# Kernel optimization log

Hardware: AMD Instinct MI355X
Metric: run time of the kernel (lower is better)

## Reference

```python
import jax, jax.numpy as jnp
import numpy as np

NUM_USERS = 100000
NUM_RATINGS = 5
EMBED_DIM = 64
ATT_DIM = 16
B, G, L, S = 16384, 8, 50, 32


def setup_inputs() -> dict:
    key = jax.random.key(0)
    ks = jax.random.split(key, 16)
    inp = {
        # forward args (int / bool constants)
        "nodes": jax.random.randint(ks[0], (B, G), 0, NUM_USERS),
        "history_u": jax.random.randint(ks[1], (B, L), 0, NUM_USERS),
        "history_r": jax.random.randint(ks[2], (B, L), 0, NUM_RATINGS),
        "history_mask": jax.random.randint(ks[3], (B, L), 0, 2).astype(bool).at[:, 0].set(True),
        "social_adj": jax.random.randint(ks[4], (B, S), 0, NUM_USERS),
        "social_mask": jax.random.randint(ks[5], (B, S), 0, 2).astype(bool).at[:, 0].set(True),
        # learned parameters
        "features": jax.random.normal(ks[6], (NUM_USERS, EMBED_DIM), jnp.float32) * 0.02,
        "r_embed": jax.random.normal(ks[7], (NUM_RATINGS, EMBED_DIM), jnp.float32) * 0.02,
        "wg1": jax.random.normal(ks[8], (EMBED_DIM, ATT_DIM), jnp.float32) / np.sqrt(EMBED_DIM),
        "bg1": jnp.zeros((ATT_DIM,), jnp.float32),
        "wg2": jax.random.normal(ks[9], (ATT_DIM, 1), jnp.float32) / np.sqrt(ATT_DIM),
        "bg2": jnp.zeros((1,), jnp.float32),
        "w1": jax.random.normal(ks[10], (2 * EMBED_DIM, EMBED_DIM), jnp.float32) / np.sqrt(2 * EMBED_DIM),
        "b1": jnp.zeros((EMBED_DIM,), jnp.float32),
    }
    return inp


def _masked_mean(x, mask):
    # x: [B, N, D], mask: [B, N] float -> [B, D]
    denom = jnp.maximum(mask.sum(axis=1, keepdims=True), 1.0)
    return (x * mask[..., None]).sum(axis=1) / denom


def reference(nodes, history_u, history_r, history_mask, social_adj, social_mask,
              features, r_embed, wg1, bg1, wg2, bg2, w1, b1):
    dt = features.dtype
    # --- Group_Embedding: attention pooling over member embeddings ---
    members = features[nodes]                              # [B, G, D] gather
    h = jnp.tanh(members @ wg1 + bg1)                      # [B, G, 16]
    logits = (h @ wg2 + bg2)[..., 0]                       # [B, G]
    alpha = jax.nn.softmax(logits, axis=-1)
    self_feats = jnp.einsum('bg,bgd->bd', alpha, members)  # [B, D]

    # --- aggregator: ragged history (item+rating) + social neighbor means ---
    hm = history_mask.astype(dt)
    hist = features[history_u] + r_embed[history_r]        # [B, L, D] gather
    hist_mean = _masked_mean(hist, hm)                     # [B, D]

    sm = social_mask.astype(dt)
    soc_mean = _masked_mean(features[social_adj], sm)      # [B, D]

    neigh_feats = 0.5 * (hist_mean + soc_mean)             # [B, D]

    # --- concat -> linear -> relu ---
    combined = jnp.concatenate([self_feats, neigh_feats], axis=1)  # [B, 2D]
    return jax.nn.relu(combined @ w1 + b1)                 # [B, D]
```

## Files before the change

### kernel.cpp

```cpp
#include <hip/hip_runtime.h>
#include <cstdint>
#include <cstddef>

#define NUSERS 100000
#define BB 16384

static __device__ __forceinline__ unsigned short f2bf(float x) {
    unsigned u = __float_as_uint(x);
    u += 0x7FFF + ((u >> 16) & 1);
    return (unsigned short)(u >> 16);
}
static __device__ __forceinline__ float4 bf4_to_f4(ushort4 h) {
    float4 r;
    r.x = __uint_as_float((unsigned)h.x << 16);
    r.y = __uint_as_float((unsigned)h.y << 16);
    r.z = __uint_as_float((unsigned)h.z << 16);
    r.w = __uint_as_float((unsigned)h.w << 16);
    return r;
}

__global__ __launch_bounds__(256) void k0_scores(
    const float* __restrict__ features, const float* __restrict__ wg1,
    const float* __restrict__ bg1, const float* __restrict__ wg2,
    const float* __restrict__ bg2, float* __restrict__ Q,
    unsigned short* __restrict__ fbf)
{
    __shared__ float frow[16 * 68];
    __shared__ float wg1t[16 * 68];
    const int tid = threadIdx.x;
    const int blk = blockIdx.x;

    const float4 v = ((const float4*)(features + (size_t)blk * 1024))[tid];
    {
        const int row = tid >> 4, q = tid & 15;
        *(float4*)&frow[row * 68 + q * 4] = v;
    }
    {
        const float4 w = ((const float4*)wg1)[tid];
        const int d = tid >> 2, k0 = (tid & 3) * 4;
        wg1t[(k0 + 0) * 68 + d] = w.x;
        wg1t[(k0 + 1) * 68 + d] = w.y;
        wg1t[(k0 + 2) * 68 + d] = w.z;
        wg1t[(k0 + 3) * 68 + d] = w.w;
    }
    {
        ushort4 o;
        o.x = f2bf(v.x); o.y = f2bf(v.y); o.z = f2bf(v.z); o.w = f2bf(v.w);
        *(ushort4*)(fbf + (size_t)blk * 1024 + tid * 4) = o;
    }
    __syncthreads();

    const int k = tid & 15, ul = tid >> 4;
    float x = bg1[k];
    #pragma unroll
    for (int d4 = 0; d4 < 16; ++d4) {
        const float4 f  = *(const float4*)&frow[ul * 68 + d4 * 4];
        const float4 wv = *(const float4*)&wg1t[k * 68 + d4 * 4];
        x += f.x * wv.x + f.y * wv.y + f.z * wv.z + f.w * wv.w;
    }
    float xx = fminf(fmaxf(x, -9.f), 9.f);
    float e2 = __expf(2.f * xx);
    float th = (e2 - 1.f) / (e2 + 1.f);
    float t = th * wg2[k];
    t += __shfl_xor(t, 1);
    t += __shfl_xor(t, 2);
    t += __shfl_xor(t, 4);
    t += __shfl_xor(t, 8);
    if (k == 0) Q[blk * 16 + ul] = t + bg2[0];
}

__global__ __launch_bounds__(256) void k1_fuse(
    const int* __restrict__ nodes, const int* __restrict__ hist_u,
    const int* __restrict__ hist_r, const int* __restrict__ hist_m,
    const int* __restrict__ soc_a, const int* __restrict__ soc_m,
    const unsigned short* __restrict__ fbf, const float* __restrict__ r_embed,
    const float* __restrict__ Q, const float* __restrict__ w1,
    const float* __restrict__ b1, float* __restrict__ out)
{
    __shared__ int   lcomp[4][96];
    __shared__ float wcomp[4][96];
    __shared__ float combs[4][128];

    const int tid = threadIdx.x;
    const int lane = tid & 63;
    const int wv = tid >> 6;
    const int e = blockIdx.x * 4 + wv;
    const int sub = lane & 15;
    const int grp = lane >> 4;
    const char* fb = (const char*)fbf;

    lcomp[wv][lane] = 0;
    wcomp[wv][lane] = 0.f;
    if (lane < 32) { lcomp[wv][64 + lane] = 0; wcomp[wv][64 + lane] = 0.f; }

    const float4* re4p = (const float4*)r_embed;
    const float4 re0 = re4p[0 * 16 + sub];
    const float4 re1 = re4p[1 * 16 + sub];
    const float4 re2 = re4p[2 * 16 + sub];
    const float4 re3 = re4p[3 * 16 + sub];
    const float4 re4 = re4p[4 * 16 + sub];

    int nd = (lane < 8) ? nodes[e * 8 + lane] : 0;
    int hu = 0, hr = 0, hmv = 0;
    if (lane < 50) {
        hu  = hist_u[e * 50 + lane];
        hr  = hist_r[e * 50 + lane];
        hmv = hist_m[e * 50 + lane];
    }
    int sa = 0, sk = 0;
    if (lane < 32) {
        sa = soc_a[e * 32 + lane];
        sk = soc_m[e * 32 + lane];
    }

    uint64_t hb = __ballot(hmv != 0);
    const int hc = (int)__popcll(hb);
    int hrank = (int)__popcll(hb & ((1ull << lane) - 1));

    uint64_t sbm = __ballot(sk != 0);
    const int scn = (int)__popcll(sbm);
    int srank = (int)__popcll(sbm & ((1ull << lane) - 1));

    const float ih = 1.f / (float)hc;
    const float is = 1.f / (float)scn;
    const float hw = 0.5f * ih;
    const float sw = 0.5f * is;

    if (hmv) { lcomp[wv][hrank] = hu << 7; wcomp[wv][hrank] = hw; }
    if (sk)  { lcomp[wv][hc + srank] = sa << 7; wcomp[wv][hc + srank] = sw; }

    const int c0 = (int)__popcll(__ballot(hmv && hr == 0));
    const int c1 = (int)__popcll(__ballot(hmv && hr == 1));
    const int c2 = (int)__popcll(__ballot(hmv && hr == 2));
    const int c3 = (int)__popcll(__ballot(hmv && hr == 3));
    const int c4 = (int)__popcll(__ballot(hmv && hr == 4));

    float sc = (lane < 8) ? Q[nd] : -1e30f;
    float mx = sc;
    mx = fmaxf(mx, __shfl_xor(mx, 1));
    mx = fmaxf(mx, __shfl_xor(mx, 2));
    mx = fmaxf(mx, __shfl_xor(mx, 4));
    float ex = __expf(sc - mx);
    float sm = ex;
    sm += __shfl_xor(sm, 1);
    sm += __shfl_xor(sm, 2);
    sm += __shfl_xor(sm, 4);
    float al = ex / sm;

    int   pkA = lcomp[wv][lane];
    int   pkB = lcomp[wv][64 + (lane & 31)];
    float wgA = wcomp[wv][lane];
    float wgB = wcomp[wv][64 + (lane & 31)];
    const int n = hc + scn;

    float4 sf4;
    {
        float a0 = __shfl(al, grp);
        int   u0 = __shfl(nd, grp);
        float a1 = __shfl(al, 4 + grp);
        int   u1 = __shfl(nd, 4 + grp);
        const float4 v0 = bf4_to_f4(*(const ushort4*)(fb + ((unsigned)u0 << 7) + sub * 8));
        const float4 v1 = bf4_to_f4(*(const ushort4*)(fb + ((unsigned)u1 << 7) + sub * 8));
        sf4.x = a0 * v0.x + a1 * v1.x;
        sf4.y = a0 * v0.y + a1 * v1.y;
        sf4.z = a0 * v0.z + a1 * v1.z;
        sf4.w = a0 * v0.w + a1 * v1.w;
    }

    float4 nb4 = {0.f, 0.f, 0.f, 0.f};
    for (int base = 0; base < n; base += 16) {
        #pragma unroll
        for (int j = 0; j < 4; ++j) {
            const int cbase = base + j * 4;
            int off; float w;
            if (cbase < 64) {
                off = __shfl(pkA, cbase + grp);
                w   = __shfl(wgA, cbase + grp);
            } else {
                off = __shfl(pkB, cbase - 64 + grp);
                w   = __shfl(wgB, cbase - 64 + grp);
            }
            const float4 v = bf4_to_f4(*(const ushort4*)(fb + (unsigned)off + sub * 8));
            nb4.x += w * v.x; nb4.y += w * v.y;
            nb4.z += w * v.z; nb4.w += w * v.w;
        }
    }

#define XRED(v4)                                            \
    v4.x += __shfl_xor(v4.x, 16); v4.x += __shfl_xor(v4.x, 32); \
    v4.y += __shfl_xor(v4.y, 16); v4.y += __shfl_xor(v4.y, 32); \
    v4.z += __shfl_xor(v4.z, 16); v4.z += __shfl_xor(v4.z, 32); \
    v4.w += __shfl_xor(v4.w, 16); v4.w += __shfl_xor(v4.w, 32);
    XRED(sf4)
    XRED(nb4)
#undef XRED

    float f0 = hw * (float)c0, f1 = hw * (float)c1, f2 = hw * (float)c2,
          f3 = hw * (float)c3, f4 = hw * (float)c4;
    nb4.x += f0 * re0.x + f1 * re1.x + f2 * re2.x + f3 * re3.x + f4 * re4.x;
    nb4.y += f0 * re0.y + f1 * re1.y + f2 * re2.y + f3 * re3.y + f4 * re4.y;
    nb4.z += f0 * re0.z + f1 * re1.z + f2 * re2.z + f3 * re3.z + f4 * re4.z;
    nb4.w += f0 * re0.w + f1 * re1.w + f2 * re2.w + f3 * re3.w + f4 * re4.w;

    if (grp == 0) *(float4*)&combs[wv][sub * 4] = sf4;
    if (grp == 1) *(float4*)&combs[wv][64 + sub * 4] = nb4;

    const int col = lane;
    float y = b1[col];
    #pragma unroll 8
    for (int k4 = 0; k4 < 32; ++k4) {
        const float4 c = *(const float4*)&combs[wv][k4 * 4];
        y += c.x * w1[(k4 * 4 + 0) * 64 + col]
           + c.y * w1[(k4 * 4 + 1) * 64 + col]
           + c.z * w1[(k4 * 4 + 2) * 64 + col]
           + c.w * w1[(k4 * 4 + 3) * 64 + col];
    }
    out[(size_t)e * 64 + col] = fmaxf(y, 0.f);
}

extern "C" void kernel_launch(void* const* d_in, const int* in_sizes, int n_in,
                              void* d_out, int out_size, void* d_ws, size_t ws_size,
                              hipStream_t stream)
{
    const int*   nodes    = (const int*)d_in[0];
    const int*   hu       = (const int*)d_in[1];
    const int*   hr       = (const int*)d_in[2];
    const int*   hm       = (const int*)d_in[3];
    const int*   sa       = (const int*)d_in[4];
    const int*   smk      = (const int*)d_in[5];
    const float* features = (const float*)d_in[6];
    const float* r_embed  = (const float*)d_in[7];
    const float* wg1      = (const float*)d_in[8];
    const float* bg1      = (const float*)d_in[9];
    const float* wg2      = (const float*)d_in[10];
    const float* bg2      = (const float*)d_in[11];
    const float* w1       = (const float*)d_in[12];
    const float* b1       = (const float*)d_in[13];
    float* out = (float*)d_out;

    float*          Q    = (float*)d_ws;
    unsigned short* fbf  = (unsigned short*)(Q + 131072);

    k0_scores<<<NUSERS / 16, 256, 0, stream>>>(features, wg1, bg1, wg2, bg2, Q, fbf);
    k1_fuse<<<BB / 4, 256, 0, stream>>>(nodes, hu, hr, hm, sa, smk,
                                        fbf, r_embed, Q, w1, b1, out);
}
```

Baseline: 139.7 us.

## Fuse score precompute into gather kernel and read fp32 features directly

```diff
diff --git a/kernel.cpp b/kernel.cpp
--- a/kernel.cpp
+++ b/kernel.cpp
@@ -2,39 +2,32 @@
 #include <cstdint>
 #include <cstddef>
 
-#define NUSERS 100000
 #define BB 16384
 
-static __device__ __forceinline__ unsigned short f2bf(float x) {
-    unsigned u = __float_as_uint(x);
-    u += 0x7FFF + ((u >> 16) & 1);
-    return (unsigned short)(u >> 16);
-}
-static __device__ __forceinline__ float4 bf4_to_f4(ushort4 h) {
-    float4 r;
-    r.x = __uint_as_float((unsigned)h.x << 16);
-    r.y = __uint_as_float((unsigned)h.y << 16);
-    r.z = __uint_as_float((unsigned)h.z << 16);
-    r.w = __uint_as_float((unsigned)h.w << 16);
-    return r;
-}
-
-__global__ __launch_bounds__(256) void k0_scores(
-    const float* __restrict__ features, const float* __restrict__ wg1,
-    const float* __restrict__ bg1, const float* __restrict__ wg2,
-    const float* __restrict__ bg2, float* __restrict__ Q,
-    unsigned short* __restrict__ fbf)
+__global__ __launch_bounds__(256) void k_fused(
+    const int* __restrict__ nodes, const int* __restrict__ hist_u,
+    const int* __restrict__ hist_r, const int* __restrict__ hist_m,
+    const int* __restrict__ soc_a, const int* __restrict__ soc_m,
+    const float* __restrict__ features, const float* __restrict__ r_embed,
+    const float* __restrict__ wg1, const float* __restrict__ bg1,
+    const float* __restrict__ wg2, const float* __restrict__ bg2,
+    const float* __restrict__ w1, const float* __restrict__ b1,
+    float* __restrict__ out)
 {
-    __shared__ float frow[16 * 68];
     __shared__ float wg1t[16 * 68];
-    const int tid = threadIdx.x;
-    const int blk = blockIdx.x;
-
-    const float4 v = ((const float4*)(features + (size_t)blk * 1024))[tid];
-    {
-        const int row = tid >> 4, q = tid & 15;
-        *(float4*)&frow[row * 68 + q * 4] = v;
-    }
+    __shared__ float mrow[4][8 * 68];
+    __shared__ int   lcomp[4][96];
+    __shared__ float wcomp[4][96];
+    __shared__ float combs[4][128];
+
+    const int tid  = threadIdx.x;
+    const int lane = tid & 63;
+    const int wv   = tid >> 6;
+    const int e    = blockIdx.x * 4 + wv;
+    const int sub  = lane & 15;
+    const int grp  = lane >> 4;
+    const char* fB = (const char*)features;
+
     {
         const float4 w = ((const float4*)wg1)[tid];
         const int d = tid >> 2, k0 = (tid & 3) * 4;
@@ -43,51 +36,6 @@
         wg1t[(k0 + 2) * 68 + d] = w.z;
         wg1t[(k0 + 3) * 68 + d] = w.w;
     }
-    {
-        ushort4 o;
-        o.x = f2bf(v.x); o.y = f2bf(v.y); o.z = f2bf(v.z); o.w = f2bf(v.w);
-        *(ushort4*)(fbf + (size_t)blk * 1024 + tid * 4) = o;
-    }
-    __syncthreads();
-
-    const int k = tid & 15, ul = tid >> 4;
-    float x = bg1[k];
-    #pragma unroll
-    for (int d4 = 0; d4 < 16; ++d4) {
-        const float4 f  = *(const float4*)&frow[ul * 68 + d4 * 4];
-        const float4 wv = *(const float4*)&wg1t[k * 68 + d4 * 4];
-        x += f.x * wv.x + f.y * wv.y + f.z * wv.z + f.w * wv.w;
-    }
-    float xx = fminf(fmaxf(x, -9.f), 9.f);
-    float e2 = __expf(2.f * xx);
-    float th = (e2 - 1.f) / (e2 + 1.f);
-    float t = th * wg2[k];
-    t += __shfl_xor(t, 1);
-    t += __shfl_xor(t, 2);
-    t += __shfl_xor(t, 4);
-    t += __shfl_xor(t, 8);
-    if (k == 0) Q[blk * 16 + ul] = t + bg2[0];
-}
-
-__global__ __launch_bounds__(256) void k1_fuse(
-    const int* __restrict__ nodes, const int* __restrict__ hist_u,
-    const int* __restrict__ hist_r, const int* __restrict__ hist_m,
-    const int* __restrict__ soc_a, const int* __restrict__ soc_m,
-    const unsigned short* __restrict__ fbf, const float* __restrict__ r_embed,
-    const float* __restrict__ Q, const float* __restrict__ w1,
-    const float* __restrict__ b1, float* __restrict__ out)
-{
-    __shared__ int   lcomp[4][96];
-    __shared__ float wcomp[4][96];
-    __shared__ float combs[4][128];
-
-    const int tid = threadIdx.x;
-    const int lane = tid & 63;
-    const int wv = tid >> 6;
-    const int e = blockIdx.x * 4 + wv;
-    const int sub = lane & 15;
-    const int grp = lane >> 4;
-    const char* fb = (const char*)fbf;
 
     lcomp[wv][lane] = 0;
     wcomp[wv][lane] = 0.f;
@@ -126,8 +74,8 @@
     const float hw = 0.5f * ih;
     const float sw = 0.5f * is;
 
-    if (hmv) { lcomp[wv][hrank] = hu << 7; wcomp[wv][hrank] = hw; }
-    if (sk)  { lcomp[wv][hc + srank] = sa << 7; wcomp[wv][hc + srank] = sw; }
+    if (hmv) { lcomp[wv][hrank] = hu << 8; wcomp[wv][hrank] = hw; }
+    if (sk)  { lcomp[wv][hc + srank] = sa << 8; wcomp[wv][hc + srank] = sw; }
 
     const int c0 = (int)__popcll(__ballot(hmv && hr == 0));
     const int c1 = (int)__popcll(__ballot(hmv && hr == 1));
@@ -135,37 +83,63 @@
     const int c3 = (int)__popcll(__ballot(hmv && hr == 3));
     const int c4 = (int)__popcll(__ballot(hmv && hr == 4));
 
-    float sc = (lane < 8) ? Q[nd] : -1e30f;
-    float mx = sc;
-    mx = fmaxf(mx, __shfl_xor(mx, 1));
-    mx = fmaxf(mx, __shfl_xor(mx, 2));
-    mx = fmaxf(mx, __shfl_xor(mx, 4));
-    float ex = __expf(sc - mx);
-    float sm = ex;
-    sm += __shfl_xor(sm, 1);
-    sm += __shfl_xor(sm, 2);
-    sm += __shfl_xor(sm, 4);
-    float al = ex / sm;
+    const int u0 = __shfl(nd, grp);
+    const int u1 = __shfl(nd, 4 + grp);
+    const float4 v0 = *(const float4*)(fB + ((unsigned)u0 << 8) + sub * 16);
+    const float4 v1 = *(const float4*)(fB + ((unsigned)u1 << 8) + sub * 16);
+    *(float4*)&mrow[wv][grp * 68 + sub * 4]       = v0;
+    *(float4*)&mrow[wv][(4 + grp) * 68 + sub * 4] = v1;
+
+    __syncthreads();
+
+    float h0, h1;
+    {
+        const int k = sub;
+        const float bk = bg1[k];
+        h0 = bk; h1 = bk;
+        #pragma unroll
+        for (int d4 = 0; d4 < 16; ++d4) {
+            const float4 wk = *(const float4*)&wg1t[k * 68 + d4 * 4];
+            const float4 m0 = *(const float4*)&mrow[wv][grp * 68 + d4 * 4];
+            const float4 m1 = *(const float4*)&mrow[wv][(4 + grp) * 68 + d4 * 4];
+            h0 += m0.x * wk.x + m0.y * wk.y + m0.z * wk.z + m0.w * wk.w;
+            h1 += m1.x * wk.x + m1.y * wk.y + m1.z * wk.z + m1.w * wk.w;
+        }
+        const float wk2 = wg2[k];
+        float x0 = fminf(fmaxf(h0, -9.f), 9.f);
+        float x1 = fminf(fmaxf(h1, -9.f), 9.f);
+        float e20 = __expf(2.f * x0), e21 = __expf(2.f * x1);
+        h0 = (e20 - 1.f) / (e20 + 1.f) * wk2;
+        h1 = (e21 - 1.f) / (e21 + 1.f) * wk2;
+        h0 += __shfl_xor(h0, 1); h1 += __shfl_xor(h1, 1);
+        h0 += __shfl_xor(h0, 2); h1 += __shfl_xor(h1, 2);
+        h0 += __shfl_xor(h0, 4); h1 += __shfl_xor(h1, 4);
+        h0 += __shfl_xor(h0, 8); h1 += __shfl_xor(h1, 8);
+    }
+    const float bg2v = bg2[0];
+    const float l0 = h0 + bg2v;
+    const float l1 = h1 + bg2v;
+
+    float mx = fmaxf(l0, l1);
+    mx = fmaxf(mx, __shfl_xor(mx, 16));
+    mx = fmaxf(mx, __shfl_xor(mx, 32));
+    float e0 = __expf(l0 - mx), e1 = __expf(l1 - mx);
+    float s = e0 + e1;
+    s += __shfl_xor(s, 16);
+    s += __shfl_xor(s, 32);
+    const float a0 = e0 / s, a1 = e1 / s;
+
+    float4 sf4;
+    sf4.x = a0 * v0.x + a1 * v1.x;
+    sf4.y = a0 * v0.y + a1 * v1.y;
+    sf4.z = a0 * v0.z + a1 * v1.z;
+    sf4.w = a0 * v0.w + a1 * v1.w;
 
     int   pkA = lcomp[wv][lane];
     int   pkB = lcomp[wv][64 + (lane & 31)];
     float wgA = wcomp[wv][lane];
     float wgB = wcomp[wv][64 + (lane & 31)];
     const int n = hc + scn;
-
-    float4 sf4;
-    {
-        float a0 = __shfl(al, grp);
-        int   u0 = __shfl(nd, grp);
-        float a1 = __shfl(al, 4 + grp);
-        int   u1 = __shfl(nd, 4 + grp);
-        const float4 v0 = bf4_to_f4(*(const ushort4*)(fb + ((unsigned)u0 << 7) + sub * 8));
-        const float4 v1 = bf4_to_f4(*(const ushort4*)(fb + ((unsigned)u1 << 7) + sub * 8));
-        sf4.x = a0 * v0.x + a1 * v1.x;
-        sf4.y = a0 * v0.y + a1 * v1.y;
-        sf4.z = a0 * v0.z + a1 * v1.z;
-        sf4.w = a0 * v0.w + a1 * v1.w;
-    }
 
     float4 nb4 = {0.f, 0.f, 0.f, 0.f};
     for (int base = 0; base < n; base += 16) {
@@ -180,7 +154,7 @@
                 off = __shfl(pkB, cbase - 64 + grp);
                 w   = __shfl(wgB, cbase - 64 + grp);
             }
-            const float4 v = bf4_to_f4(*(const ushort4*)(fb + (unsigned)off + sub * 8));
+            const float4 v = *(const float4*)(fB + (unsigned)off + sub * 16);
             nb4.x += w * v.x; nb4.y += w * v.y;
             nb4.z += w * v.z; nb4.w += w * v.w;
         }
@@ -238,10 +212,9 @@
     const float* b1       = (const float*)d_in[13];
     float* out = (float*)d_out;
 
-    float*          Q    = (float*)d_ws;
-    unsigned short* fbf  = (unsigned short*)(Q + 131072);
-
-    k0_scores<<<NUSERS / 16, 256, 0, stream>>>(features, wg1, bg1, wg2, bg2, Q, fbf);
-    k1_fuse<<<BB / 4, 256, 0, stream>>>(nodes, hu, hr, hm, sa, smk,
-                                        fbf, r_embed, Q, w1, b1, out);
+    (void)d_ws; (void)ws_size;
+
+    k_fused<<<BB / 4, 256, 0, stream>>>(nodes, hu, hr, hm, sa, smk,
+                                        features, r_embed, wg1, bg1, wg2, bg2,
+                                        w1, b1, out);
 }
```

After: 140.3 us. Within noise of the previous version (+0.4%).

## Cut LDS and registers in fused kernel, vectorize final linear with float4 w1

Applied to the files above, without the earlier changes.

```diff
diff --git a/kernel.cpp b/kernel.cpp
--- a/kernel.cpp
+++ b/kernel.cpp
@@ -77,28 +77,21 @@
     const float* __restrict__ Q, const float* __restrict__ w1,
     const float* __restrict__ b1, float* __restrict__ out)
 {
-    __shared__ int   lcomp[4][96];
-    __shared__ float wcomp[4][96];
-    __shared__ float combs[4][128];
-
-    const int tid = threadIdx.x;
+    __shared__ float wvbuf[4][128];
+
+    const int tid  = threadIdx.x;
     const int lane = tid & 63;
-    const int wv = tid >> 6;
-    const int e = blockIdx.x * 4 + wv;
-    const int sub = lane & 15;
-    const int grp = lane >> 4;
+    const int wv   = tid >> 6;
+    const int e    = blockIdx.x * 4 + wv;
+    const int sub  = lane & 15;
+    const int grp  = lane >> 4;
     const char* fb = (const char*)fbf;
 
-    lcomp[wv][lane] = 0;
-    wcomp[wv][lane] = 0.f;
-    if (lane < 32) { lcomp[wv][64 + lane] = 0; wcomp[wv][64 + lane] = 0.f; }
-
-    const float4* re4p = (const float4*)r_embed;
-    const float4 re0 = re4p[0 * 16 + sub];
-    const float4 re1 = re4p[1 * 16 + sub];
-    const float4 re2 = re4p[2 * 16 + sub];
-    const float4 re3 = re4p[3 * 16 + sub];
-    const float4 re4 = re4p[4 * 16 + sub];
+    int*   lc = (int*)&wvbuf[wv][0];
+    float* cb = &wvbuf[wv][0];
+
+    lc[lane] = 0;
+    if (lane < 32) lc[64 + lane] = 0;
 
     int nd = (lane < 8) ? nodes[e * 8 + lane] : 0;
     int hu = 0, hr = 0, hmv = 0;
@@ -121,19 +114,21 @@
     const int scn = (int)__popcll(sbm);
     int srank = (int)__popcll(sbm & ((1ull << lane) - 1));
 
-    const float ih = 1.f / (float)hc;
-    const float is = 1.f / (float)scn;
-    const float hw = 0.5f * ih;
-    const float sw = 0.5f * is;
-
-    if (hmv) { lcomp[wv][hrank] = hu << 7; wcomp[wv][hrank] = hw; }
-    if (sk)  { lcomp[wv][hc + srank] = sa << 7; wcomp[wv][hc + srank] = sw; }
+    const float hw = 0.5f / (float)hc;
+    const float sw = 0.5f / (float)scn;
+    const int   n  = hc + scn;
+
+    if (hmv) lc[hrank] = hu << 7;
+    if (sk)  lc[hc + srank] = sa << 7;
 
     const int c0 = (int)__popcll(__ballot(hmv && hr == 0));
     const int c1 = (int)__popcll(__ballot(hmv && hr == 1));
     const int c2 = (int)__popcll(__ballot(hmv && hr == 2));
     const int c3 = (int)__popcll(__ballot(hmv && hr == 3));
     const int c4 = (int)__popcll(__ballot(hmv && hr == 4));
+
+    int pkA = lc[lane];
+    int pkB = lc[64 + (lane & 31)];
 
     float sc = (lane < 8) ? Q[nd] : -1e30f;
     float mx = sc;
@@ -147,18 +142,12 @@
     sm += __shfl_xor(sm, 4);
     float al = ex / sm;
 
-    int   pkA = lcomp[wv][lane];
-    int   pkB = lcomp[wv][64 + (lane & 31)];
-    float wgA = wcomp[wv][lane];
-    float wgB = wcomp[wv][64 + (lane & 31)];
-    const int n = hc + scn;
-
     float4 sf4;
     {
-        float a0 = __shfl(al, grp);
-        int   u0 = __shfl(nd, grp);
-        float a1 = __shfl(al, 4 + grp);
-        int   u1 = __shfl(nd, 4 + grp);
+        const float a0 = __shfl(al, grp);
+        const int   u0 = __shfl(nd, grp);
+        const float a1 = __shfl(al, 4 + grp);
+        const int   u1 = __shfl(nd, 4 + grp);
         const float4 v0 = bf4_to_f4(*(const ushort4*)(fb + ((unsigned)u0 << 7) + sub * 8));
         const float4 v1 = bf4_to_f4(*(const ushort4*)(fb + ((unsigned)u1 << 7) + sub * 8));
         sf4.x = a0 * v0.x + a1 * v1.x;
@@ -172,14 +161,11 @@
         #pragma unroll
         for (int j = 0; j < 4; ++j) {
             const int cbase = base + j * 4;
-            int off; float w;
-            if (cbase < 64) {
-                off = __shfl(pkA, cbase + grp);
-                w   = __shfl(wgA, cbase + grp);
-            } else {
-                off = __shfl(pkB, cbase - 64 + grp);
-                w   = __shfl(wgB, cbase - 64 + grp);
-            }
+            int off;
+            if (cbase < 64) off = __shfl(pkA, cbase + grp);
+            else            off = __shfl(pkB, cbase - 64 + grp);
+            const int idx = cbase + grp;
+            const float w = (idx < hc) ? hw : ((idx < n) ? sw : 0.f);
             const float4 v = bf4_to_f4(*(const ushort4*)(fb + (unsigned)off + sub * 8));
             nb4.x += w * v.x; nb4.y += w * v.y;
             nb4.z += w * v.z; nb4.w += w * v.w;
@@ -195,27 +181,47 @@
     XRED(nb4)
 #undef XRED
 
-    float f0 = hw * (float)c0, f1 = hw * (float)c1, f2 = hw * (float)c2,
-          f3 = hw * (float)c3, f4 = hw * (float)c4;
-    nb4.x += f0 * re0.x + f1 * re1.x + f2 * re2.x + f3 * re3.x + f4 * re4.x;
-    nb4.y += f0 * re0.y + f1 * re1.y + f2 * re2.y + f3 * re3.y + f4 * re4.y;
-    nb4.z += f0 * re0.z + f1 * re1.z + f2 * re2.z + f3 * re3.z + f4 * re4.z;
-    nb4.w += f0 * re0.w + f1 * re1.w + f2 * re2.w + f3 * re3.w + f4 * re4.w;
-
-    if (grp == 0) *(float4*)&combs[wv][sub * 4] = sf4;
-    if (grp == 1) *(float4*)&combs[wv][64 + sub * 4] = nb4;
-
-    const int col = lane;
-    float y = b1[col];
+    {
+        const float4* re4p = (const float4*)r_embed;
+        const float4 re0 = re4p[0 * 16 + sub];
+        const float4 re1 = re4p[1 * 16 + sub];
+        const float4 re2 = re4p[2 * 16 + sub];
+        const float4 re3 = re4p[3 * 16 + sub];
+        const float4 re4 = re4p[4 * 16 + sub];
+        float f0 = hw * (float)c0, f1 = hw * (float)c1, f2 = hw * (float)c2,
+              f3 = hw * (float)c3, f4 = hw * (float)c4;
+        nb4.x += f0 * re0.x + f1 * re1.x + f2 * re2.x + f3 * re3.x + f4 * re4.x;
+        nb4.y += f0 * re0.y + f1 * re1.y + f2 * re2.y + f3 * re3.y + f4 * re4.y;
+        nb4.z += f0 * re0.z + f1 * re1.z + f2 * re2.z + f3 * re3.z + f4 * re4.z;
+        nb4.w += f0 * re0.w + f1 * re1.w + f2 * re2.w + f3 * re3.w + f4 * re4.w;
+    }
+
+    if (grp == 0) *(float4*)&cb[sub * 4] = sf4;
+    if (grp == 1) *(float4*)&cb[64 + sub * 4] = nb4;
+
+    float4 p = {0.f, 0.f, 0.f, 0.f};
     #pragma unroll 8
-    for (int k4 = 0; k4 < 32; ++k4) {
-        const float4 c = *(const float4*)&combs[wv][k4 * 4];
-        y += c.x * w1[(k4 * 4 + 0) * 64 + col]
-           + c.y * w1[(k4 * 4 + 1) * 64 + col]
-           + c.z * w1[(k4 * 4 + 2) * 64 + col]
-           + c.w * w1[(k4 * 4 + 3) * 64 + col];
-    }
-    out[(size_t)e * 64 + col] = fmaxf(y, 0.f);
+    for (int j = 0; j < 32; ++j) {
+        const float  c   = cb[j * 4 + grp];
+        const float4 wv4 = *(const float4*)(w1 + (j * 4 + grp) * 64 + sub * 4);
+        p.x += c * wv4.x;
+        p.y += c * wv4.y;
+        p.z += c * wv4.z;
+        p.w += c * wv4.w;
+    }
+    p.x += __shfl_xor(p.x, 16); p.x += __shfl_xor(p.x, 32);
+    p.y += __shfl_xor(p.y, 16); p.y += __shfl_xor(p.y, 32);
+    p.z += __shfl_xor(p.z, 16); p.z += __shfl_xor(p.z, 32);
+    p.w += __shfl_xor(p.w, 16); p.w += __shfl_xor(p.w, 32);
+    if (grp == 0) {
+        const float4 bv = *(const float4*)(b1 + sub * 4);
+        float4 o;
+        o.x = fmaxf(p.x + bv.x, 0.f);
+        o.y = fmaxf(p.y + bv.y, 0.f);
+        o.z = fmaxf(p.z + bv.z, 0.f);
+        o.w = fmaxf(p.w + bv.w, 0.f);
+        *(float4*)(out + (size_t)e * 64 + sub * 4) = o;
+    }
 }
 
 extern "C" void kernel_launch(void* const* d_in, const int* in_sizes, int n_in,
@@ -238,8 +244,8 @@
     const float* b1       = (const float*)d_in[13];
     float* out = (float*)d_out;
 
-    float*          Q    = (float*)d_ws;
-    unsigned short* fbf  = (unsigned short*)(Q + 131072);
+    float*          Q   = (float*)d_ws;
+    unsigned short* fbf = (unsigned short*)(Q + 131072);
 
     k0_scores<<<NUSERS / 16, 256, 0, stream>>>(features, wg1, bg1, wg2, bg2, Q, fbf);
     k1_fuse<<<BB / 4, 256, 0, stream>>>(nodes, hu, hr, hm, sa, smk,
```

Result: no change. 138.5 us (-0.8%).
